# Optimization experiments

Measured on AMD Instinct MI355X. Metric: run time of the kernel, lower is better.

The kernel has to match this reference:

```python
import jax, jax.numpy as jnp
import numpy as np

VOCAB = 128000
DIM = 2048
Q_MIN, Q_MAX = -128.0, 127.0  # int8 quantization mode range


def quantize_weights(w):
    # Snap weights (already living in the quantized value range) onto the int grid.
    return jnp.clip(jnp.round(w), Q_MIN, Q_MAX)


def dynamically_quantize_activations(x):
    # Dynamic absmax int8 fake-quantization of activations.
    scale = jnp.max(jnp.abs(x)) / Q_MAX
    scale = jnp.maximum(scale, jnp.asarray(1e-12, x.dtype))
    q = jnp.clip(jnp.round(x / scale), Q_MIN, Q_MAX)
    return q * scale


def setup_inputs() -> dict:
    key = jax.random.key(0)
    k1, k2, k3, k4 = jax.random.split(key, 4)
    weights = jax.random.uniform(k1, (VOCAB, DIM), minval=Q_MIN, maxval=Q_MAX, dtype=jnp.float32)
    scales = jax.random.uniform(k2, (VOCAB,), minval=0.5, maxval=1.5, dtype=jnp.float32)
    tokens = jax.random.randint(k3, (8192,), 0, VOCAB, dtype=jnp.int32)
    x = jax.random.normal(k4, (DIM,), dtype=jnp.float32)
    return {"weights": weights, "scales": scales, "tokens": tokens, "x": x}


def reference(weights, scales, tokens, x):
    # prepare_weights: dequantized (quantize -> per-row scale) full table
    prepared = quantize_weights(weights) * scales[:, None]  # [vocab, dim]
    # embed: gather rows
    embed_out = prepared[tokens]  # [tokens, dim]
    # readout: dynamic activation quantization then GEMV
    xq = dynamically_quantize_activations(x)
    readout_out = prepared @ xq  # [vocab]
    return embed_out, readout_out
```

## Files before the change

### kernel.cpp

```cpp
#include <hip/hip_runtime.h>

#define VOCAB 128000
#define DIM 2048
#define NTOK 8192

#define EMB_BLOCKS NTOK
#define RO_BLOCKS (VOCAB / 4)

__device__ __forceinline__ float qclip(float w) {
  return fminf(fmaxf(rintf(w), -128.0f), 127.0f);
}

__global__ __launch_bounds__(256) void fused_qembed_kernel(
    const float* __restrict__ W, const float* __restrict__ scales,
    const int* __restrict__ tokens, const float* __restrict__ x,
    float* __restrict__ out_embed, float* __restrict__ out_readout) {
  const int b = blockIdx.x;

  if (b < EMB_BLOCKS) {
    const int t = b;
    const int tok = tokens[t];
    const float s = scales[tok];
    const float4* __restrict__ wrow =
        reinterpret_cast<const float4*>(W + (size_t)tok * DIM);
    float4* __restrict__ orow =
        reinterpret_cast<float4*>(out_embed + (size_t)t * DIM);
    #pragma unroll
    for (int k = 0; k < DIM / 4 / 256; ++k) {
      const int i = threadIdx.x + k * 256;
      float4 w4 = wrow[i];
      float4 r;
      r.x = qclip(w4.x) * s;
      r.y = qclip(w4.y) * s;
      r.z = qclip(w4.z) * s;
      r.w = qclip(w4.w) * s;
      orow[i] = r;
    }
    return;
  }

  const int rb = b - EMB_BLOCKS;
  const int wid = threadIdx.x >> 6;
  const int lane = threadIdx.x & 63;
  const int row = rb * 4 + wid;

  const float4* __restrict__ xv = reinterpret_cast<const float4*>(x);
  float4 xl[8];
  float m = 0.0f;
  #pragma unroll
  for (int k = 0; k < 8; ++k) {
    xl[k] = xv[lane + k * 64];
    m = fmaxf(m, fmaxf(fmaxf(fabsf(xl[k].x), fabsf(xl[k].y)),
                       fmaxf(fabsf(xl[k].z), fabsf(xl[k].w))));
  }
  #pragma unroll
  for (int off = 32; off > 0; off >>= 1) m = fmaxf(m, __shfl_xor(m, off, 64));
  const float scale = fmaxf(m / 127.0f, 1e-12f);
  const float rcp = 1.0f / scale;

  #pragma unroll
  for (int k = 0; k < 8; ++k) {
    xl[k].x = fminf(fmaxf(rintf(xl[k].x * rcp), -128.0f), 127.0f) * scale;
    xl[k].y = fminf(fmaxf(rintf(xl[k].y * rcp), -128.0f), 127.0f) * scale;
    xl[k].z = fminf(fmaxf(rintf(xl[k].z * rcp), -128.0f), 127.0f) * scale;
    xl[k].w = fminf(fmaxf(rintf(xl[k].w * rcp), -128.0f), 127.0f) * scale;
  }

  const float4* __restrict__ wrow =
      reinterpret_cast<const float4*>(W + (size_t)row * DIM);
  float acc = 0.0f;
  #pragma unroll
  for (int k = 0; k < 8; ++k) {
    float4 w4 = wrow[lane + k * 64];
    acc += qclip(w4.x) * xl[k].x;
    acc += qclip(w4.y) * xl[k].y;
    acc += qclip(w4.z) * xl[k].z;
    acc += qclip(w4.w) * xl[k].w;
  }
  #pragma unroll
  for (int off = 32; off > 0; off >>= 1) acc += __shfl_down(acc, off, 64);
  if (lane == 0) out_readout[row] = acc * scales[row];
}

extern "C" void kernel_launch(void* const* d_in, const int* in_sizes, int n_in,
                              void* d_out, int out_size, void* d_ws, size_t ws_size,
                              hipStream_t stream) {
  const float* W      = (const float*)d_in[0];
  const float* scales = (const float*)d_in[1];
  const int*   tokens = (const int*)d_in[2];
  const float* x      = (const float*)d_in[3];

  float* out_embed   = (float*)d_out;
  float* out_readout = (float*)d_out + (size_t)NTOK * DIM;

  fused_qembed_kernel<<<EMB_BLOCKS + RO_BLOCKS, 256, 0, stream>>>(
      W, scales, tokens, x, out_embed, out_readout);
}
```

Before: 200.8 us.

## Fuse embedding gather into readout GEMV via per-row token linked lists

Builds per-vocab-row linked lists of token indices with atomicExch in workspace. The readout kernel then writes each loaded, quantized row to every output position that gathers it. This removes the separate re-read of gathered weight rows and reuses the row already held in registers. In exchange it adds two small extra kernel launches and serial per-warp stores for duplicate tokens. It keeps a fallback kernel when the workspace is too small.

Measured after the change: 223.3 us. 1.11x slower.

```diff
diff --git a/kernel.cpp b/kernel.cpp
--- a/kernel.cpp
+++ b/kernel.cpp
@@ -3,30 +3,116 @@
 #define VOCAB 128000
 #define DIM 2048
 #define NTOK 8192
-
-#define EMB_BLOCKS NTOK
 #define RO_BLOCKS (VOCAB / 4)
 
 __device__ __forceinline__ float qclip(float w) {
   return fminf(fmaxf(rintf(w), -128.0f), 127.0f);
 }
 
-__global__ __launch_bounds__(256) void fused_qembed_kernel(
+__global__ __launch_bounds__(256) void init_heads_kernel(int* __restrict__ head) {
+  const int i = blockIdx.x * 256 + threadIdx.x;
+  if (i < VOCAB) head[i] = -1;
+}
+
+__global__ __launch_bounds__(256) void build_lists_kernel(
+    const int* __restrict__ tokens, int* __restrict__ head,
+    int* __restrict__ next) {
+  const int t = blockIdx.x * 256 + threadIdx.x;
+  if (t < NTOK) {
+    const int row = tokens[t];
+    next[t] = atomicExch(&head[row], t);
+  }
+}
+
+__global__ __launch_bounds__(256) void fused_readout_embed_kernel(
+    const float* __restrict__ W, const float* __restrict__ scales,
+    const float* __restrict__ x, const int* __restrict__ head,
+    const int* __restrict__ next, float* __restrict__ out_embed,
+    float* __restrict__ out_readout) {
+  const int wid = threadIdx.x >> 6;
+  const int lane = threadIdx.x & 63;
+  const int row = blockIdx.x * 4 + wid;
+
+  const float4* __restrict__ xv = reinterpret_cast<const float4*>(x);
+  const float4* __restrict__ wrow =
+      reinterpret_cast<const float4*>(W + (size_t)row * DIM);
+
+  float4 xl[8];
+  #pragma unroll
+  for (int k = 0; k < 8; ++k) xl[k] = xv[lane + k * 64];
+
+  float4 wq[8];
+  #pragma unroll
+  for (int k = 0; k < 8; ++k) wq[k] = wrow[lane + k * 64];
+
+  const int tok0 = head[row];
+
+  float m = 0.0f;
+  #pragma unroll
+  for (int k = 0; k < 8; ++k) {
+    m = fmaxf(m, fmaxf(fmaxf(fabsf(xl[k].x), fabsf(xl[k].y)),
+                       fmaxf(fabsf(xl[k].z), fabsf(xl[k].w))));
+  }
+  #pragma unroll
+  for (int off = 32; off > 0; off >>= 1) m = fmaxf(m, __shfl_xor(m, off, 64));
+  const float scale = fmaxf(m / 127.0f, 1e-12f);
+  const float rcp = 1.0f / scale;
+  #pragma unroll
+  for (int k = 0; k < 8; ++k) {
+    xl[k].x = fminf(fmaxf(rintf(xl[k].x * rcp), -128.0f), 127.0f) * scale;
+    xl[k].y = fminf(fmaxf(rintf(xl[k].y * rcp), -128.0f), 127.0f) * scale;
+    xl[k].z = fminf(fmaxf(rintf(xl[k].z * rcp), -128.0f), 127.0f) * scale;
+    xl[k].w = fminf(fmaxf(rintf(xl[k].w * rcp), -128.0f), 127.0f) * scale;
+  }
+
+  float acc = 0.0f;
+  #pragma unroll
+  for (int k = 0; k < 8; ++k) {
+    wq[k].x = qclip(wq[k].x);
+    wq[k].y = qclip(wq[k].y);
+    wq[k].z = qclip(wq[k].z);
+    wq[k].w = qclip(wq[k].w);
+    acc += wq[k].x * xl[k].x;
+    acc += wq[k].y * xl[k].y;
+    acc += wq[k].z * xl[k].z;
+    acc += wq[k].w * xl[k].w;
+  }
+  #pragma unroll
+  for (int off = 32; off > 0; off >>= 1) acc += __shfl_down(acc, off, 64);
+  const float srow = scales[row];
+  if (lane == 0) out_readout[row] = acc * srow;
+
+  int t = tok0;
+  while (t >= 0) {
+    float4* __restrict__ orow =
+        reinterpret_cast<float4*>(out_embed + (size_t)t * DIM);
+    #pragma unroll
+    for (int k = 0; k < 8; ++k) {
+      float4 r;
+      r.x = wq[k].x * srow;
+      r.y = wq[k].y * srow;
+      r.z = wq[k].z * srow;
+      r.w = wq[k].w * srow;
+      orow[lane + k * 64] = r;
+    }
+    t = next[t];
+  }
+}
+
+__global__ __launch_bounds__(256) void fallback_fused_kernel(
     const float* __restrict__ W, const float* __restrict__ scales,
     const int* __restrict__ tokens, const float* __restrict__ x,
     float* __restrict__ out_embed, float* __restrict__ out_readout) {
   const int b = blockIdx.x;
-
-  if (b < EMB_BLOCKS) {
-    const int t = b;
-    const int tok = tokens[t];
+  if (b < NTOK) {
+    const int tok = tokens[b];
     const float s = scales[tok];
     const float4* __restrict__ wrow =
         reinterpret_cast<const float4*>(W + (size_t)tok * DIM);
     float4* __restrict__ orow =
-        reinterpret_cast<float4*>(out_embed + (size_t)t * DIM);
+        reinterpret_cast<float4*>(out_embed + (size_t)b * DIM);
     #pragma unroll
-    for (int k = 0; k < DIM / 4 / 256; ++k) {
+    for (int k = 0; k < 2; ++k) {
       const int i = threadIdx.x + k * 256;
       float4 w4 = wrow[i];
       float4 r;
@@ -38,12 +124,10 @@
     }
     return;
   }
-
-  const int rb = b - EMB_BLOCKS;
+  const int rb = b - NTOK;
   const int wid = threadIdx.x >> 6;
   const int lane = threadIdx.x & 63;
   const int row = rb * 4 + wid;
-
   const float4* __restrict__ xv = reinterpret_cast<const float4*>(x);
   float4 xl[8];
   float m = 0.0f;
@@ -57,7 +141,6 @@
   for (int off = 32; off > 0; off >>= 1) m = fmaxf(m, __shfl_xor(m, off, 64));
   const float scale = fmaxf(m / 127.0f, 1e-12f);
   const float rcp = 1.0f / scale;
-
   #pragma unroll
   for (int k = 0; k < 8; ++k) {
     xl[k].x = fminf(fmaxf(rintf(xl[k].x * rcp), -128.0f), 127.0f) * scale;
@@ -65,7 +148,6 @@
     xl[k].z = fminf(fmaxf(rintf(xl[k].z * rcp), -128.0f), 127.0f) * scale;
     xl[k].w = fminf(fmaxf(rintf(xl[k].w * rcp), -128.0f), 127.0f) * scale;
   }
-
   const float4* __restrict__ wrow =
       reinterpret_cast<const float4*>(W + (size_t)row * DIM);
   float acc = 0.0f;
@@ -93,6 +175,16 @@
   float* out_embed   = (float*)d_out;
   float* out_readout = (float*)d_out + (size_t)NTOK * DIM;
 
-  fused_qembed_kernel<<<EMB_BLOCKS + RO_BLOCKS, 256, 0, stream>>>(
-      W, scales, tokens, x, out_embed, out_readout);
+  const size_t need = (size_t)(VOCAB + NTOK) * sizeof(int);
+  if (ws_size >= need) {
+    int* head = (int*)d_ws;
+    int* next = head + VOCAB;
+    init_heads_kernel<<<(VOCAB + 255) / 256, 256, 0, stream>>>(head);
+    build_lists_kernel<<<(NTOK + 255) / 256, 256, 0, stream>>>(tokens, head, next);
+    fused_readout_embed_kernel<<<RO_BLOCKS, 256, 0, stream>>>(
+        W, scales, x, head, next, out_embed, out_readout);
+  } else {
+    fallback_fused_kernel<<<NTOK + RO_BLOCKS, 256, 0, stream>>>(
+        W, scales, tokens, x, out_embed, out_readout);
+  }
 }
```
